# Kernel optimization log

Hardware: AMD Instinct MI355X
Metric: run time of the kernel (lower is better)

The kernel has to match this reference:

```python
import jax, jax.numpy as jnp
import numpy as np

DIM = 256
HEADS = 8
HEAD_DIM = DIM // HEADS
SCALE = HEAD_DIM ** -0.5
EPS = 1e-5


def layer_norm(x, w, b):
    mu = jnp.mean(x, axis=-1, keepdims=True)
    var = jnp.mean(jnp.square(x - mu), axis=-1, keepdims=True)
    return (x - mu) * jax.lax.rsqrt(var + EPS) * w + b


def setup_inputs() -> dict:
    key = jax.random.key(0)
    ks = jax.random.split(key, 12)
    B, C, H, W = 2, DIM, 64, 64
    q_feat = jax.random.normal(ks[0], (B, C, H, W), dtype=jnp.float32)
    kv_feat = jax.random.normal(ks[1], (B, C, H, W), dtype=jnp.float32)
    s = 0.02
    return {
        "q_feat": q_feat,
        "kv_feat": kv_feat,
        "norm_q_w": jnp.ones((C,), jnp.float32),
        "norm_q_b": jnp.zeros((C,), jnp.float32),
        "norm_kv_w": jnp.ones((C,), jnp.float32),
        "norm_kv_b": jnp.zeros((C,), jnp.float32),
        "wq": jax.random.normal(ks[2], (C, C), jnp.float32) * s,
        "bq": jnp.zeros((C,), jnp.float32),
        "wk": jax.random.normal(ks[3], (C, C), jnp.float32) * s,
        "bk": jnp.zeros((C,), jnp.float32),
        "wv": jax.random.normal(ks[4], (C, C), jnp.float32) * s,
        "bv": jnp.zeros((C,), jnp.float32),
        "wp": jax.random.normal(ks[5], (C, C), jnp.float32) * s,
        "bp": jnp.zeros((C,), jnp.float32),
    }


def reference(q_feat, kv_feat, norm_q_w, norm_q_b, norm_kv_w, norm_kv_b,
              wq, bq, wk, bk, wv, bv, wp, bp):
    B, C, H, W = q_feat.shape
    N = H * W
    # N > max_tokens(256) -> avg_pool2d(k=2,s=2) on kv (H,W even so no ceil padding)
    kv = kv_feat.reshape(B, C, H // 2, 2, W // 2, 2).mean(axis=(3, 5))
    Hk, Wk = kv.shape[2], kv.shape[3]
    Nk = Hk * Wk
    q = q_feat.transpose(0, 2, 3, 1).reshape(B, N, C)
    kv = kv.transpose(0, 2, 3, 1).reshape(B, Nk, C)
    q = layer_norm(q, norm_q_w, norm_q_b)
    kv = layer_norm(kv, norm_kv_w, norm_kv_b)
    # projections (weights stored as (out,in) like torch Linear: x @ W.T + b)
    qh = (q @ wq.T + bq).reshape(B, N, HEADS, HEAD_DIM).transpose(0, 2, 1, 3)
    kh = (kv @ wk.T + bk).reshape(B, Nk, HEADS, HEAD_DIM).transpose(0, 2, 1, 3)
    vh = (kv @ wv.T + bv).reshape(B, Nk, HEADS, HEAD_DIM).transpose(0, 2, 1, 3)
    attn = jnp.einsum("bhnd,bhmd->bhnm", qh * SCALE, kh)
    attn = jax.nn.softmax(attn, axis=-1)
    out = jnp.einsum("bhnm,bhmd->bhnd", attn, vh)
    out = out.transpose(0, 2, 1, 3).reshape(B, N, C)
    out = out @ wp.T + bp
    return out.reshape(B, H, W, C).transpose(0, 3, 1, 2)
```

## Files before the change

### kernel.cpp

```cpp
#include <hip/hip_runtime.h>


#define CDIM   256
#define NTOK   4096
#define NKTOK  1024
#define HDIM   32
#define QSCALE 0.2550530290582177f
#define LN_EPS 1e-5f

typedef __attribute__((ext_vector_type(8))) short bf16x8;
typedef __attribute__((ext_vector_type(4))) float f32x4;
typedef __attribute__((ext_vector_type(4))) uint u32x4;

__device__ __forceinline__ ushort f2bf(float f) {
  uint u = __builtin_bit_cast(uint, f);
  u += 0x7fff + ((u >> 16) & 1);
  return (ushort)(u >> 16);
}

__device__ __forceinline__ float fast_exp2(float x) {
  float r;
  asm("v_exp_f32 %0, %1" : "=v"(r) : "v"(x));
  return r;
}

__device__ __forceinline__ uint cvt_pk_bf16(float lo, float hi) {
  uint r;
  asm("v_cvt_pk_bf16_f32 %0, %1, %2" : "=v"(r) : "v"(lo), "v"(hi));
  return r;
}

__device__ __forceinline__ void gload_lds16(const void* g, void* l) {
  __builtin_amdgcn_global_load_lds(
      (const __attribute__((address_space(1))) unsigned int*)g,
      (__attribute__((address_space(3))) unsigned int*)l, 16, 0, 0);
}

__global__ __launch_bounds__(256) void prep_kernel(
    const float* __restrict__ q_feat, const float* __restrict__ kv_feat,
    const float* __restrict__ nqw, const float* __restrict__ nqb,
    const float* __restrict__ nkw, const float* __restrict__ nkb,
    const float* __restrict__ wq, const float* __restrict__ wk,
    const float* __restrict__ wvv, const float* __restrict__ wp,
    ushort* __restrict__ wq_bf, ushort* __restrict__ wk_bf,
    ushort* __restrict__ wv_bf, ushort* __restrict__ wp_bf,
    ushort* __restrict__ q_ln, ushort* __restrict__ kv_ln) {
  __shared__ float preds[2][256];
  __shared__ float pstat[2][32];
  const int bid = blockIdx.x;
  const int tid = threadIdx.x;

  if (bid < 256) {
    const int mat = bid >> 6;
    const int base = (bid & 63) * 1024 + tid * 4;
    const float* s; ushort* d;
    switch (mat) {
      case 0: s = wq; d = wq_bf; break;
      case 1: s = wk; d = wk_bf; break;
      case 2: s = wvv; d = wv_bf; break;
      default: s = wp; d = wp_bf; break;
    }
    const float4 v = *reinterpret_cast<const float4*>(s + base);
    uint2 pk;
    pk.x = (uint)f2bf(v.x) | ((uint)f2bf(v.y) << 16);
    pk.y = (uint)f2bf(v.z) | ((uint)f2bf(v.w) << 16);
    *reinterpret_cast<uint2*>(d + base) = pk;
    return;
  }

  if (bid < 768) {
    const int tok = tid & 15, cg = tid >> 4;
    const int T = (bid - 256) * 16 + tok;
    const int b = T >> 12, n = T & 4095;
    const float* src = q_feat + ((size_t)b * CDIM + cg * 16) * NTOK + n;
    float vals[16];
    float s = 0.f, ss = 0.f;
#pragma unroll
    for (int ci = 0; ci < 16; ++ci) {
      const float v = src[(size_t)ci * NTOK];
      vals[ci] = v;
      s += v; ss = fmaf(v, v, ss);
    }
    preds[0][cg * 16 + tok] = s;
    preds[1][cg * 16 + tok] = ss;
    __syncthreads();
    if (tid < 16) {
      float st = 0.f, sst = 0.f;
#pragma unroll
      for (int k = 0; k < 16; ++k) { st += preds[0][k * 16 + tid]; sst += preds[1][k * 16 + tid]; }
      const float mu = st * (1.f / 256.f);
      const float var = sst * (1.f / 256.f) - mu * mu;
      pstat[0][tid] = mu;
      pstat[1][tid] = rsqrtf(var + LN_EPS);
    }
    __syncthreads();
    const float mu = pstat[0][tok];
    const float rs = pstat[1][tok];
    ushort* dst = q_ln + (size_t)T * CDIM + cg * 16;
#pragma unroll
    for (int ci = 0; ci < 16; ci += 4) {
      ushort h[4];
#pragma unroll
      for (int j = 0; j < 4; ++j) {
        const int c = cg * 16 + ci + j;
        h[j] = f2bf(fmaf((vals[ci + j] - mu) * rs, nqw[c], nqb[c]));
      }
      uint2 pk;
      pk.x = (uint)h[0] | ((uint)h[1] << 16);
      pk.y = (uint)h[2] | ((uint)h[3] << 16);
      *reinterpret_cast<uint2*>(dst + ci) = pk;
    }
    return;
  }

  {
    const int tok = tid & 7, cg = tid >> 3;
    const int T = (bid - 768) * 8 + tok;
    const int b = T >> 10, nk = T & 1023;
    const int hk = nk >> 5, wk2 = nk & 31;
    const float* src = kv_feat + ((size_t)b * CDIM + cg * 8) * NTOK + hk * 128 + wk2 * 2;
    float vals[8];
    float s = 0.f, ss = 0.f;
#pragma unroll
    for (int ci = 0; ci < 8; ++ci) {
      const float* p = src + (size_t)ci * NTOK;
      const float2 r0 = *reinterpret_cast<const float2*>(p);
      const float2 r1 = *reinterpret_cast<const float2*>(p + 64);
      const float v = 0.25f * ((r0.x + r0.y) + (r1.x + r1.y));
      vals[ci] = v;
      s += v; ss = fmaf(v, v, ss);
    }
    preds[0][cg * 8 + tok] = s;
    preds[1][cg * 8 + tok] = ss;
    __syncthreads();
    if (tid < 8) {
      float st = 0.f, sst = 0.f;
#pragma unroll
      for (int k = 0; k < 32; ++k) { st += preds[0][k * 8 + tid]; sst += preds[1][k * 8 + tid]; }
      const float mu = st * (1.f / 256.f);
      const float var = sst * (1.f / 256.f) - mu * mu;
      pstat[0][tid] = mu;
      pstat[1][tid] = rsqrtf(var + LN_EPS);
    }
    __syncthreads();
    const float mu = pstat[0][tok];
    const float rs = pstat[1][tok];
    ushort* dst = kv_ln + (size_t)T * CDIM + cg * 8;
#pragma unroll
    for (int ci = 0; ci < 8; ci += 4) {
      ushort h[4];
#pragma unroll
      for (int j = 0; j < 4; ++j) {
        const int c = cg * 8 + ci + j;
        h[j] = f2bf(fmaf((vals[ci + j] - mu) * rs, nkw[c], nkb[c]));
      }
      uint2 pk;
      pk.x = (uint)h[0] | ((uint)h[1] << 16);
      pk.y = (uint)h[2] | ((uint)h[3] << 16);
      *reinterpret_cast<uint2*>(dst + ci) = pk;
    }
  }
}

__global__ __launch_bounds__(256) void qkv_kernel(
    const ushort* __restrict__ q_ln, const ushort* __restrict__ kv_ln,
    const ushort* __restrict__ wq_bf, const ushort* __restrict__ wk_bf,
    const ushort* __restrict__ wv_bf,
    const float* __restrict__ bq, const float* __restrict__ bk,
    const float* __restrict__ bv,
    ushort* __restrict__ Qp, ushort* __restrict__ Kp, ushort* __restrict__ Vt) {
  const int bid = blockIdx.x;
  int seg, sb;
  const ushort *X, *W; const float* bias;
  if (bid < 256)      { seg = 0; sb = bid;       X = q_ln;  W = wq_bf; bias = bq; }
  else if (bid < 320) { seg = 1; sb = bid - 256; X = kv_ln; W = wk_bf; bias = bk; }
  else                { seg = 2; sb = bid - 320; X = kv_ln; W = wv_bf; bias = bv; }

  const int lane = threadIdx.x & 63;
  const int wvi = threadIdx.x >> 6;
  const int nlan = lane & 15, g = lane >> 4;
  const int rowgrp = wvi >> 1, colh = wvi & 1;
  const int r0 = sb * 32 + rowgrp * 16;

  f32x4 acc[8];
#pragma unroll
  for (int nt = 0; nt < 8; ++nt) acc[nt] = (f32x4){0.f, 0.f, 0.f, 0.f};

  const ushort* xp = X + (size_t)(r0 + nlan) * CDIM + g * 8;
  const ushort* wp = W + (size_t)(colh * 128 + nlan) * CDIM + g * 8;
#pragma unroll
  for (int k0 = 0; k0 < 8; ++k0) {
    const bf16x8 a = *reinterpret_cast<const bf16x8*>(xp + k0 * 32);
#pragma unroll
    for (int nt = 0; nt < 8; ++nt) {
      const bf16x8 bfr = *reinterpret_cast<const bf16x8*>(wp + (size_t)nt * 16 * CDIM + k0 * 32);
      acc[nt] = __builtin_amdgcn_mfma_f32_16x16x32_bf16(a, bfr, acc[nt], 0, 0, 0);
    }
  }

#pragma unroll
  for (int nt = 0; nt < 8; ++nt) {
    const int j = colh * 128 + nt * 16 + nlan;
    const float bj = bias[j];
#pragma unroll
    for (int reg = 0; reg < 4; ++reg) {
      const int r = r0 + 4 * g + reg;
      const float v = acc[nt][reg] + bj;
      if (seg == 0) {
        Qp[(size_t)r * CDIM + j] = f2bf(v * QSCALE);
      } else if (seg == 1) {
        Kp[(size_t)r * CDIM + j] = f2bf(v);
      } else {
        const int h = j >> 5, d = j & 31;
        const int bb = r >> 10, m = r & 1023;
        Vt[((size_t)((bb * 8 + h) * 32 + d)) * NKTOK + m] = f2bf(v);
      }
    }
  }
}

__global__ __launch_bounds__(256) void attn_kernel(const ushort* __restrict__ Qp,
                                                   const ushort* __restrict__ Kp,
                                                   const ushort* __restrict__ Vt,
                                                   ushort* __restrict__ aout) {
  __shared__ __align__(16) ushort kvf[2][16][512];
  const int lane = threadIdx.x & 63;
  const int wvi = threadIdx.x >> 6;
  const int nlan = lane & 15, g = lane >> 4;
  const int bh = blockIdx.y;
  const int b = bh >> 3, h = bh & 7;
  const int n0 = blockIdx.x * 128 + wvi * 32;

  bf16x8 qf[2];
#pragma unroll
  for (int qt = 0; qt < 2; ++qt)
    qf[qt] = *reinterpret_cast<const bf16x8*>(
        Qp + (size_t)(b * NTOK + n0 + qt * 16 + nlan) * CDIM + h * HDIM + g * 8);

  const ushort* kb = Kp + (size_t)b * NKTOK * CDIM + h * HDIM;
  const ushort* vb = Vt + (size_t)(b * 8 + h) * HDIM * NKTOK;

  auto stage = [&](int buf, int kc) {
#pragma unroll
    for (int i = 0; i < 4; ++i) {
      const int t = wvi * 4 + i;
      const ushort* src;
      if (t < 8) {
        const int krow = kc + (t >> 1) * 32 + (nlan >> 2) * 8 + (t & 1) * 4 + (nlan & 3);
        src = kb + (size_t)krow * CDIM + g * 8;
      } else {
        const int j = t - 8, dt = j >> 2, ks = j & 3;
        src = vb + (size_t)(dt * 16 + nlan) * NKTOK + kc + ks * 32 + g * 8;
      }
      gload_lds16(src, &kvf[buf][t][0]);
    }
  };

  f32x4 acc[2][2];
#pragma unroll
  for (int qt = 0; qt < 2; ++qt) {
    acc[qt][0] = (f32x4){0.f, 0.f, 0.f, 0.f};
    acc[qt][1] = (f32x4){0.f, 0.f, 0.f, 0.f};
  }
  float lsum[2] = {0.f, 0.f};
  const f32x4 zero = {0.f, 0.f, 0.f, 0.f};

  stage(0, 0);
  for (int c = 0; c < 8; ++c) {
    const int buf = c & 1;
    __syncthreads();
    if (c < 7) stage(buf ^ 1, (c + 1) * 128);

#pragma unroll
    for (int m = 0; m < 4; ++m) {
      uint pk[2][4];
#pragma unroll
      for (int half = 0; half < 2; ++half) {
        const bf16x8 kf = *reinterpret_cast<const bf16x8*>(&kvf[buf][2 * m + half][lane * 8]);
#pragma unroll
        for (int qt = 0; qt < 2; ++qt) {
          const f32x4 s = __builtin_amdgcn_mfma_f32_16x16x32_bf16(kf, qf[qt], zero, 0, 0, 0);
          const float p0 = fast_exp2(s[0]), p1 = fast_exp2(s[1]);
          const float p2 = fast_exp2(s[2]), p3 = fast_exp2(s[3]);
          lsum[qt] += (p0 + p1) + (p2 + p3);
          pk[qt][half * 2 + 0] = cvt_pk_bf16(p0, p1);
          pk[qt][half * 2 + 1] = cvt_pk_bf16(p2, p3);
        }
      }
      bf16x8 af[2];
#pragma unroll
      for (int qt = 0; qt < 2; ++qt) {
        const u32x4 w = {pk[qt][0], pk[qt][1], pk[qt][2], pk[qt][3]};
        af[qt] = __builtin_bit_cast(bf16x8, w);
      }
#pragma unroll
      for (int dt = 0; dt < 2; ++dt) {
        const bf16x8 vf = *reinterpret_cast<const bf16x8*>(&kvf[buf][8 + dt * 4 + m][lane * 8]);
#pragma unroll
        for (int qt = 0; qt < 2; ++qt)
          acc[qt][dt] = __builtin_amdgcn_mfma_f32_16x16x32_bf16(af[qt], vf, acc[qt][dt], 0, 0, 0);
      }
    }
  }

#pragma unroll
  for (int qt = 0; qt < 2; ++qt) {
    lsum[qt] += __shfl_xor(lsum[qt], 16);
    lsum[qt] += __shfl_xor(lsum[qt], 32);
  }

  ushort* dst = aout + (size_t)(b * NTOK + n0) * CDIM + h * HDIM;
#pragma unroll
  for (int qt = 0; qt < 2; ++qt) {
#pragma unroll
    for (int reg = 0; reg < 4; ++reg) {
      const float inv = 1.f / __shfl(lsum[qt], 4 * g + reg);
      const size_t row = (size_t)(qt * 16 + 4 * g + reg) * CDIM;
      dst[row + nlan] = f2bf(acc[qt][0][reg] * inv);
      dst[row + 16 + nlan] = f2bf(acc[qt][1][reg] * inv);
    }
  }
}

__global__ __launch_bounds__(256) void outproj_kernel(const ushort* __restrict__ A,
                                                      const ushort* __restrict__ W,
                                                      const float* __restrict__ bias,
                                                      float* __restrict__ out) {
  __shared__ float ts[256][33];
  const int lane = threadIdx.x & 63;
  const int wvi = threadIdx.x >> 6;
  const int nlan = lane & 15, g = lane >> 4;
  const int rowgrp = wvi >> 1, colh = wvi & 1;
  const int r0b = blockIdx.x * 32;
  const int r0 = r0b + rowgrp * 16;

  f32x4 acc[8];
#pragma unroll
  for (int nt = 0; nt < 8; ++nt) acc[nt] = (f32x4){0.f, 0.f, 0.f, 0.f};

  const ushort* xp = A + (size_t)(r0 + nlan) * CDIM + g * 8;
  const ushort* wp = W + (size_t)(colh * 128 + nlan) * CDIM + g * 8;
#pragma unroll
  for (int k0 = 0; k0 < 8; ++k0) {
    const bf16x8 a = *reinterpret_cast<const bf16x8*>(xp + k0 * 32);
#pragma unroll
    for (int nt = 0; nt < 8; ++nt) {
      const bf16x8 bfr = *reinterpret_cast<const bf16x8*>(wp + (size_t)nt * 16 * CDIM + k0 * 32);
      acc[nt] = __builtin_amdgcn_mfma_f32_16x16x32_bf16(a, bfr, acc[nt], 0, 0, 0);
    }
  }

#pragma unroll
  for (int nt = 0; nt < 8; ++nt) {
    const int j = colh * 128 + nt * 16 + nlan;
    const float bj = bias[j];
#pragma unroll
    for (int reg = 0; reg < 4; ++reg)
      ts[j][rowgrp * 16 + 4 * g + reg] = acc[nt][reg] + bj;
  }
  __syncthreads();
  const int b = r0b >> 12;
  const int n0g = r0b & 4095;
#pragma unroll
  for (int k = 0; k < 32; ++k) {
    const int idx = k * 256 + threadIdx.x;
    const int cl = idx >> 5, tok = idx & 31;
    out[((size_t)b * CDIM + cl) * NTOK + n0g + tok] = ts[cl][tok];
  }
}

extern "C" void kernel_launch(void* const* d_in, const int* in_sizes, int n_in,
                              void* d_out, int out_size, void* d_ws, size_t ws_size,
                              hipStream_t stream) {
  (void)in_sizes; (void)n_in; (void)out_size; (void)ws_size;
  const float* q_feat  = (const float*)d_in[0];
  const float* kv_feat = (const float*)d_in[1];
  const float* nqw = (const float*)d_in[2];
  const float* nqb = (const float*)d_in[3];
  const float* nkw = (const float*)d_in[4];
  const float* nkb = (const float*)d_in[5];
  const float* wq  = (const float*)d_in[6];
  const float* bq  = (const float*)d_in[7];
  const float* wk  = (const float*)d_in[8];
  const float* bk  = (const float*)d_in[9];
  const float* wv  = (const float*)d_in[10];
  const float* bv  = (const float*)d_in[11];
  const float* wp  = (const float*)d_in[12];
  const float* bp  = (const float*)d_in[13];
  float* out = (float*)d_out;

  ushort* p = (ushort*)d_ws;
  ushort* wq_bf = p; p += 65536;
  ushort* wk_bf = p; p += 65536;
  ushort* wv_bf = p; p += 65536;
  ushort* wp_bf = p; p += 65536;
  ushort* q_ln  = p; p += 8192 * 256;
  ushort* kv_ln = p; p += 2048 * 256;
  ushort* Qp    = p; p += 8192 * 256;
  ushort* Kp    = p; p += 2048 * 256;
  ushort* Vt    = p; p += 2048 * 256;
  ushort* aout  = p; p += 8192 * 256;

  prep_kernel<<<1024, 256, 0, stream>>>(q_feat, kv_feat, nqw, nqb, nkw, nkb,
                                        wq, wk, wv, wp,
                                        wq_bf, wk_bf, wv_bf, wp_bf, q_ln, kv_ln);
  qkv_kernel<<<384, 256, 0, stream>>>(q_ln, kv_ln, wq_bf, wk_bf, wv_bf,
                                      bq, bk, bv, Qp, Kp, Vt);
  attn_kernel<<<dim3(32, 16), 256, 0, stream>>>(Qp, Kp, Vt, aout);
  outproj_kernel<<<256, 256, 0, stream>>>(aout, wp_bf, bp, out);
}
```

Baseline: 64.98 us.

## Load K/V fragments directly into registers with register double-buffering instead of LDS

The attention kernel no longer stages K and V tiles through shared memory with global_load_lds and __syncthreads. Each wave now loads its own K/V MFMA fragments straight from global memory into registers, double-buffered across chunks so loads overlap compute. This removes LDS traffic and block barriers, but every wave redundantly fetches the same K/V data (four times more global/L2 reads) and register pressure grows.

```diff
diff --git a/kernel.cpp b/kernel.cpp
--- a/kernel.cpp
+++ b/kernel.cpp
@@ -28,12 +28,6 @@
   uint r;
   asm("v_cvt_pk_bf16_f32 %0, %1, %2" : "=v"(r) : "v"(lo), "v"(hi));
   return r;
-}
-
-__device__ __forceinline__ void gload_lds16(const void* g, void* l) {
-  __builtin_amdgcn_global_load_lds(
-      (const __attribute__((address_space(1))) unsigned int*)g,
-      (__attribute__((address_space(3))) unsigned int*)l, 16, 0, 0);
 }
 
 __global__ __launch_bounds__(256) void prep_kernel(
@@ -223,7 +217,6 @@
                                                    const ushort* __restrict__ Kp,
                                                    const ushort* __restrict__ Vt,
                                                    ushort* __restrict__ aout) {
-  __shared__ __align__(16) ushort kvf[2][16][512];
   const int lane = threadIdx.x & 63;
   const int wvi = threadIdx.x >> 6;
   const int nlan = lane & 15, g = lane >> 4;
@@ -237,24 +230,10 @@
     qf[qt] = *reinterpret_cast<const bf16x8*>(
         Qp + (size_t)(b * NTOK + n0 + qt * 16 + nlan) * CDIM + h * HDIM + g * 8);
 
-  const ushort* kb = Kp + (size_t)b * NKTOK * CDIM + h * HDIM;
-  const ushort* vb = Vt + (size_t)(b * 8 + h) * HDIM * NKTOK;
-
-  auto stage = [&](int buf, int kc) {
-#pragma unroll
-    for (int i = 0; i < 4; ++i) {
-      const int t = wvi * 4 + i;
-      const ushort* src;
-      if (t < 8) {
-        const int krow = kc + (t >> 1) * 32 + (nlan >> 2) * 8 + (t & 1) * 4 + (nlan & 3);
-        src = kb + (size_t)krow * CDIM + g * 8;
-      } else {
-        const int j = t - 8, dt = j >> 2, ks = j & 3;
-        src = vb + (size_t)(dt * 16 + nlan) * NKTOK + kc + ks * 32 + g * 8;
-      }
-      gload_lds16(src, &kvf[buf][t][0]);
-    }
-  };
+  const ushort* kfb = Kp + (size_t)b * NKTOK * CDIM + h * HDIM +
+                      (size_t)((nlan >> 2) * 8 + (nlan & 3)) * CDIM + g * 8;
+  const ushort* vfb = Vt + (size_t)(b * 8 + h) * HDIM * NKTOK +
+                      (size_t)nlan * NKTOK + g * 8;
 
   f32x4 acc[2][2];
 #pragma unroll
@@ -265,18 +244,24 @@
   float lsum[2] = {0.f, 0.f};
   const f32x4 zero = {0.f, 0.f, 0.f, 0.f};
 
-  stage(0, 0);
-  for (int c = 0; c < 8; ++c) {
-    const int buf = c & 1;
-    __syncthreads();
-    if (c < 7) stage(buf ^ 1, (c + 1) * 128);
-
+  auto load_chunk = [&](bf16x8 (&KR)[8], bf16x8 (&VR)[8], int kc) {
+#pragma unroll
+    for (int t = 0; t < 8; ++t)
+      KR[t] = *reinterpret_cast<const bf16x8*>(
+          kfb + (size_t)(kc + (t >> 1) * 32 + (t & 1) * 4) * CDIM);
+#pragma unroll
+    for (int j = 0; j < 8; ++j)
+      VR[j] = *reinterpret_cast<const bf16x8*>(
+          vfb + (size_t)(j >> 2) * 16 * NKTOK + kc + (j & 3) * 32);
+  };
+
+  auto compute_chunk = [&](const bf16x8 (&KR)[8], const bf16x8 (&VR)[8]) {
 #pragma unroll
     for (int m = 0; m < 4; ++m) {
       uint pk[2][4];
 #pragma unroll
       for (int half = 0; half < 2; ++half) {
-        const bf16x8 kf = *reinterpret_cast<const bf16x8*>(&kvf[buf][2 * m + half][lane * 8]);
+        const bf16x8 kf = KR[2 * m + half];
 #pragma unroll
         for (int qt = 0; qt < 2; ++qt) {
           const f32x4 s = __builtin_amdgcn_mfma_f32_16x16x32_bf16(kf, qf[qt], zero, 0, 0, 0);
@@ -287,20 +272,25 @@
           pk[qt][half * 2 + 1] = cvt_pk_bf16(p2, p3);
         }
       }
-      bf16x8 af[2];
 #pragma unroll
       for (int qt = 0; qt < 2; ++qt) {
         const u32x4 w = {pk[qt][0], pk[qt][1], pk[qt][2], pk[qt][3]};
-        af[qt] = __builtin_bit_cast(bf16x8, w);
+        const bf16x8 af = __builtin_bit_cast(bf16x8, w);
+#pragma unroll
+        for (int dt = 0; dt < 2; ++dt)
+          acc[qt][dt] = __builtin_amdgcn_mfma_f32_16x16x32_bf16(af, VR[dt * 4 + m], acc[qt][dt], 0, 0, 0);
       }
-#pragma unroll
-      for (int dt = 0; dt < 2; ++dt) {
-        const bf16x8 vf = *reinterpret_cast<const bf16x8*>(&kvf[buf][8 + dt * 4 + m][lane * 8]);
-#pragma unroll
-        for (int qt = 0; qt < 2; ++qt)
-          acc[qt][dt] = __builtin_amdgcn_mfma_f32_16x16x32_bf16(af[qt], vf, acc[qt][dt], 0, 0, 0);
-      }
-    }
+    }
+  };
+
+  bf16x8 KA[8], VA[8], KB[8], VB[8];
+  load_chunk(KA, VA, 0);
+#pragma unroll
+  for (int c = 0; c < 8; c += 2) {
+    load_chunk(KB, VB, (c + 1) * 128);
+    compute_chunk(KA, VA);
+    if (c + 2 < 8) load_chunk(KA, VA, (c + 2) * 128);
+    compute_chunk(KB, VB);
   }
 
 #pragma unroll
```

Measured after the change: 87.18 us. 34.2% more time.

## Pre-swizzle K and V into tile-contiguous layout for attention staging

Applied to the files above, without the earlier changes.

The QKV projection now writes K and V straight into a packed buffer already ordered per (batch, head, chunk, tile) in the exact layout the attention kernel copies into LDS. Each staging load then becomes one contiguous 1 KB read per tile instead of strided row gathers. The aim is fewer memory transactions and less address arithmetic in the attention inner loop. In exchange the projection epilogue does scattered 2-byte stores with more index math, and the PV MFMA loop is reordered to loop over query tiles first.

```diff
diff --git a/kernel.cpp b/kernel.cpp
--- a/kernel.cpp
+++ b/kernel.cpp
@@ -168,7 +168,7 @@
     const ushort* __restrict__ wv_bf,
     const float* __restrict__ bq, const float* __restrict__ bk,
     const float* __restrict__ bv,
-    ushort* __restrict__ Qp, ushort* __restrict__ Kp, ushort* __restrict__ Vt) {
+    ushort* __restrict__ Qp, ushort* __restrict__ kvp) {
   const int bid = blockIdx.x;
   int seg, sb;
   const ushort *X, *W; const float* bias;
@@ -209,19 +209,30 @@
       if (seg == 0) {
         Qp[(size_t)r * CDIM + j] = f2bf(v * QSCALE);
       } else if (seg == 1) {
-        Kp[(size_t)r * CDIM + j] = f2bf(v);
+        const int bb = r >> 10, k = r & 1023;
+        const int kc = k >> 7, kk = k & 127;
+        const int m = kk >> 5, w = kk & 31;
+        const int t = 2 * m + ((w >> 2) & 1);
+        const int rr = ((w >> 3) << 2) | (w & 3);
+        const int hh = j >> 5, d = j & 31;
+        kvp[(((size_t)((bb * 8 + hh) * 8 + kc) * 16 + t) << 9) +
+            ((d >> 3) * 16 + rr) * 8 + (d & 7)] = f2bf(v);
       } else {
-        const int h = j >> 5, d = j & 31;
-        const int bb = r >> 10, m = r & 1023;
-        Vt[((size_t)((bb * 8 + h) * 32 + d)) * NKTOK + m] = f2bf(v);
+        const int bb = r >> 10, mk = r & 1023;
+        const int hh = j >> 5, d = j & 31;
+        const int dt = d >> 4, rr = d & 15;
+        const int kc = mk >> 7, km = mk & 127;
+        const int ks = km >> 5, w = km & 31;
+        const int gq = w >> 3, jj = w & 7;
+        kvp[(((size_t)((bb * 8 + hh) * 8 + kc) * 16 + (8 + dt * 4 + ks)) << 9) +
+            (gq * 16 + rr) * 8 + jj] = f2bf(v);
       }
     }
   }
 }
 
 __global__ __launch_bounds__(256) void attn_kernel(const ushort* __restrict__ Qp,
-                                                   const ushort* __restrict__ Kp,
-                                                   const ushort* __restrict__ Vt,
+                                                   const ushort* __restrict__ kvp,
                                                    ushort* __restrict__ aout) {
   __shared__ __align__(16) ushort kvf[2][16][512];
   const int lane = threadIdx.x & 63;
@@ -237,22 +248,14 @@
     qf[qt] = *reinterpret_cast<const bf16x8*>(
         Qp + (size_t)(b * NTOK + n0 + qt * 16 + nlan) * CDIM + h * HDIM + g * 8);
 
-  const ushort* kb = Kp + (size_t)b * NKTOK * CDIM + h * HDIM;
-  const ushort* vb = Vt + (size_t)(b * 8 + h) * HDIM * NKTOK;
-
-  auto stage = [&](int buf, int kc) {
+  const ushort* kvb = kvp + ((size_t)bh << 16);
+
+  auto stage = [&](int buf, int kc_idx) {
+    const ushort* cb = kvb + ((size_t)kc_idx << 13);
 #pragma unroll
     for (int i = 0; i < 4; ++i) {
       const int t = wvi * 4 + i;
-      const ushort* src;
-      if (t < 8) {
-        const int krow = kc + (t >> 1) * 32 + (nlan >> 2) * 8 + (t & 1) * 4 + (nlan & 3);
-        src = kb + (size_t)krow * CDIM + g * 8;
-      } else {
-        const int j = t - 8, dt = j >> 2, ks = j & 3;
-        src = vb + (size_t)(dt * 16 + nlan) * NKTOK + kc + ks * 32 + g * 8;
-      }
-      gload_lds16(src, &kvf[buf][t][0]);
+      gload_lds16(cb + t * 512 + lane * 8, &kvf[buf][t][0]);
     }
   };
 
@@ -269,7 +272,7 @@
   for (int c = 0; c < 8; ++c) {
     const int buf = c & 1;
     __syncthreads();
-    if (c < 7) stage(buf ^ 1, (c + 1) * 128);
+    if (c < 7) stage(buf ^ 1, c + 1);
 
 #pragma unroll
     for (int m = 0; m < 4; ++m) {
@@ -287,18 +290,15 @@
           pk[qt][half * 2 + 1] = cvt_pk_bf16(p2, p3);
         }
       }
-      bf16x8 af[2];
 #pragma unroll
       for (int qt = 0; qt < 2; ++qt) {
         const u32x4 w = {pk[qt][0], pk[qt][1], pk[qt][2], pk[qt][3]};
-        af[qt] = __builtin_bit_cast(bf16x8, w);
-      }
-#pragma unroll
-      for (int dt = 0; dt < 2; ++dt) {
-        const bf16x8 vf = *reinterpret_cast<const bf16x8*>(&kvf[buf][8 + dt * 4 + m][lane * 8]);
-#pragma unroll
-        for (int qt = 0; qt < 2; ++qt)
-          acc[qt][dt] = __builtin_amdgcn_mfma_f32_16x16x32_bf16(af[qt], vf, acc[qt][dt], 0, 0, 0);
+        const bf16x8 af = __builtin_bit_cast(bf16x8, w);
+#pragma unroll
+        for (int dt = 0; dt < 2; ++dt) {
+          const bf16x8 vf = *reinterpret_cast<const bf16x8*>(&kvf[buf][8 + dt * 4 + m][lane * 8]);
+          acc[qt][dt] = __builtin_amdgcn_mfma_f32_16x16x32_bf16(af, vf, acc[qt][dt], 0, 0, 0);
+        }
       }
     }
   }
@@ -397,15 +397,14 @@
   ushort* q_ln  = p; p += 8192 * 256;
   ushort* kv_ln = p; p += 2048 * 256;
   ushort* Qp    = p; p += 8192 * 256;
-  ushort* Kp    = p; p += 2048 * 256;
-  ushort* Vt    = p; p += 2048 * 256;
+  ushort* kvp   = p; p += 16 * 8 * 16 * 512;
   ushort* aout  = p; p += 8192 * 256;
 
   prep_kernel<<<1024, 256, 0, stream>>>(q_feat, kv_feat, nqw, nqb, nkw, nkb,
                                         wq, wk, wv, wp,
                                         wq_bf, wk_bf, wv_bf, wp_bf, q_ln, kv_ln);
   qkv_kernel<<<384, 256, 0, stream>>>(q_ln, kv_ln, wq_bf, wk_bf, wv_bf,
-                                      bq, bk, bv, Qp, Kp, Vt);
-  attn_kernel<<<dim3(32, 16), 256, 0, stream>>>(Qp, Kp, Vt, aout);
+                                      bq, bk, bv, Qp, kvp);
+  attn_kernel<<<dim3(32, 16), 256, 0, stream>>>(Qp, kvp, aout);
   outproj_kernel<<<256, 256, 0, stream>>>(aout, wp_bf, bp, out);
 }
```

After: 62.16 us. -4.3%, faster.
